# Kernel tuning notes

Measured on AMD Instinct MI355X. Metric: run time of the kernel, lower is better.

Reference implementation:

```python
import jax, jax.numpy as jnp
import numpy as np
import math

B, H, S, D = 4, 16, 1024, 64
NEG = -1000000000.0

def setup_inputs() -> dict:
    key = jax.random.key(0)
    ks = jax.random.split(key, 6)
    return {
        "query": jax.random.normal(ks[0], (B, H, S, D), dtype=jnp.float32),
        "key": jax.random.normal(ks[1], (B, H, S, D), dtype=jnp.float32),
        "value": jax.random.normal(ks[2], (B, H, S, D), dtype=jnp.float32),
        "head_nums": H,
        "mask": jax.random.randint(ks[3], (B, S), 0, 2, dtype=jnp.int32),
        "topic_query": jax.random.normal(ks[4], (B, S, D), dtype=jnp.float32),
        "topic_key": jax.random.normal(ks[5], (B, S, D), dtype=jnp.float32),
    }

def reference(query, key, value, head_nums, mask, topic_query, topic_key):
    d = query.shape[-1]
    # scores: [B,H,S,S]
    scores = jnp.einsum("bhqd,bhkd->bhqk", query, key) / math.sqrt(d)
    # pairwise mask: [B,S,S] (mask_i * mask_j)
    pair_mask = (mask[:, :, None] * mask[:, None, :]) != 0
    scores = jnp.where(pair_mask[:, None, :, :], scores, NEG)
    # topic modulation: per-token (no head dim), broadcast over heads
    dt = topic_query.shape[-1]
    topic_scores = jnp.einsum("bqd,bkd->bqk", topic_query, topic_key) / math.sqrt(dt)
    topic_scores = jnp.where(pair_mask, topic_scores, 1.0)[:, None, :, :]  # [B,1,S,S]
    topic_probs = jax.nn.softmax(topic_scores, axis=-1)
    scores = scores * topic_probs
    p_attn = jax.nn.softmax(scores, axis=-1)
    out = jnp.einsum("bhqk,bhkd->bhqd", p_attn, value)
    return (out, p_attn)
```

## Files before the change

### kernel.cpp

```cpp
#include <hip/hip_runtime.h>

#define B_ 4
#define H_ 16
#define S_ 1024
#define D_ 64
#define NEGV -1000000000.0f

typedef __bf16 bf16x8 __attribute__((ext_vector_type(8)));
typedef float f32x4 __attribute__((ext_vector_type(4)));

__global__ __launch_bounds__(256) void prep_kernel(
    const float* __restrict__ K, const float* __restrict__ V,
    __bf16* __restrict__ Kb, __bf16* __restrict__ Vt)
{
  int bid = blockIdx.x;
  int sc = bid & 15;
  int bh = bid >> 4;
  int tid = threadIdx.x;
  __shared__ float s_v[64][65];

  const float* Kc = K + ((size_t)bh*S_ + sc*64)*D_;
  const float* Vc = V + ((size_t)bh*S_ + sc*64)*D_;
  __bf16* Kbc = Kb + ((size_t)bh*S_ + sc*64)*D_;

  {
    const float4* src = (const float4*)Kc + tid*4;
    float4 a = src[0], b = src[1], c = src[2], d = src[3];
    bf16x8 o0, o1;
    o0[0]=(__bf16)a.x; o0[1]=(__bf16)a.y; o0[2]=(__bf16)a.z; o0[3]=(__bf16)a.w;
    o0[4]=(__bf16)b.x; o0[5]=(__bf16)b.y; o0[6]=(__bf16)b.z; o0[7]=(__bf16)b.w;
    o1[0]=(__bf16)c.x; o1[1]=(__bf16)c.y; o1[2]=(__bf16)c.z; o1[3]=(__bf16)c.w;
    o1[4]=(__bf16)d.x; o1[5]=(__bf16)d.y; o1[6]=(__bf16)d.z; o1[7]=(__bf16)d.w;
    *(bf16x8*)(Kbc + tid*16)     = o0;
    *(bf16x8*)(Kbc + tid*16 + 8) = o1;
  }
  for (int i = tid; i < 64*16; i += 256) {
    int r = i >> 4, c4 = i & 15;
    float4 v = ((const float4*)(Vc + (size_t)r*D_))[c4];
    s_v[r][c4*4+0] = v.x; s_v[r][c4*4+1] = v.y;
    s_v[r][c4*4+2] = v.z; s_v[r][c4*4+3] = v.w;
  }
  __syncthreads();
  {
    int d = tid >> 2, seg = tid & 3;
    bf16x8 o0, o1;
    #pragma unroll
    for (int j = 0; j < 8; ++j) o0[j] = (__bf16)s_v[seg*16 + j][d];
    #pragma unroll
    for (int j = 0; j < 8; ++j) o1[j] = (__bf16)s_v[seg*16 + 8 + j][d];
    __bf16* dst = Vt + ((size_t)bh*D_ + d)*S_ + sc*64 + seg*16;
    *(bf16x8*)dst = o0;
    *(bf16x8*)(dst + 8) = o1;
  }
}

__global__ __launch_bounds__(256) void topic_kernel(
    const float* __restrict__ tq, const float* __restrict__ tk,
    const int* __restrict__ mask, float* __restrict__ tp)
{
  int bid = blockIdx.x;
  int qt = bid & 63, b = bid >> 6;
  int tid = threadIdx.x;
  int wave = tid >> 6, lane = tid & 63;
  int l15 = lane & 15, lhi = lane >> 4;

  __shared__ float s_t[16*1024];

  bf16x8 qf[2];
  #pragma unroll
  for (int dc = 0; dc < 2; ++dc) {
    const float* p = tq + ((size_t)b*S_ + qt*16 + l15)*D_ + dc*32 + lhi*8;
    float4 x = *(const float4*)p;
    float4 y = *(const float4*)(p+4);
    bf16x8 f;
    f[0]=(__bf16)x.x; f[1]=(__bf16)x.y; f[2]=(__bf16)x.z; f[3]=(__bf16)x.w;
    f[4]=(__bf16)y.x; f[5]=(__bf16)y.y; f[6]=(__bf16)y.z; f[7]=(__bf16)y.w;
    qf[dc] = f;
  }
  int mq[4];
  #pragma unroll
  for (int i = 0; i < 4; ++i) mq[i] = mask[b*S_ + qt*16 + lhi*4 + i];

  for (int kt = 0; kt < 16; ++kt) {
    int kb = wave*256 + kt*16;
    int kcol = kb + l15;
    f32x4 acc = {0.f,0.f,0.f,0.f};
    #pragma unroll
    for (int dc = 0; dc < 2; ++dc) {
      const float* p = tk + ((size_t)b*S_ + kcol)*D_ + dc*32 + lhi*8;
      float4 x = *(const float4*)p;
      float4 y = *(const float4*)(p+4);
      bf16x8 f;
      f[0]=(__bf16)x.x; f[1]=(__bf16)x.y; f[2]=(__bf16)x.z; f[3]=(__bf16)x.w;
      f[4]=(__bf16)y.x; f[5]=(__bf16)y.y; f[6]=(__bf16)y.z; f[7]=(__bf16)y.w;
      acc = __builtin_amdgcn_mfma_f32_16x16x32_bf16(qf[dc], f, acc, 0, 0, 0);
    }
    int mk = mask[b*S_ + kcol];
    #pragma unroll
    for (int i = 0; i < 4; ++i) {
      int row = lhi*4 + i;
      float s = (mq[i] && mk) ? acc[i]*0.125f : 1.0f;
      s_t[row*1024 + (kcol ^ ((row&7)<<2))] = s;
    }
  }
  __syncthreads();

  int mkv[16];
  #pragma unroll
  for (int j = 0; j < 16; ++j) mkv[j] = mask[b*S_ + lane + j*64];
  int mqr[4];
  #pragma unroll
  for (int r = 0; r < 4; ++r) mqr[r] = mask[b*S_ + qt*16 + wave*4 + r];

  #pragma unroll
  for (int r = 0; r < 4; ++r) {
    int row = wave*4 + r;
    int swz = (row & 7) << 2;
    float sv[16]; float m = -3.4e38f;
    #pragma unroll
    for (int j = 0; j < 16; ++j) {
      sv[j] = s_t[row*1024 + ((lane + j*64) ^ swz)];
      m = fmaxf(m, sv[j]);
    }
    #pragma unroll
    for (int o = 32; o >= 1; o >>= 1) m = fmaxf(m, __shfl_xor(m, o));
    float ev[16]; float sum = 0.f;
    #pragma unroll
    for (int j = 0; j < 16; ++j) { ev[j] = __expf(sv[j]-m); sum += ev[j]; }
    #pragma unroll
    for (int o = 32; o >= 1; o >>= 1) sum += __shfl_xor(sum, o);
    float inv = 1.0f/sum;
    float* tpr = tp + ((size_t)b*S_ + qt*16 + row)*S_;
    #pragma unroll
    for (int j = 0; j < 16; ++j) {
      float p = ev[j]*inv;
      tpr[lane + j*64] = (mqr[r] && mkv[j]) ? p : -p;
    }
  }
}

__global__ __launch_bounds__(256) void attn_kernel(
    const float* __restrict__ Q, const __bf16* __restrict__ Kb,
    const __bf16* __restrict__ Vt, const float* __restrict__ tp,
    float* __restrict__ out, float* __restrict__ pa)
{
  int bid0 = blockIdx.x;
  int bid = (bid0 & 7)*512 + (bid0 >> 3);
  int qt = bid & 63;
  int h  = (bid >> 6) & 15;
  int b  = bid >> 10;
  int tid = threadIdx.x;
  int wave = tid >> 6, lane = tid & 63;
  int l15 = lane & 15, lhi = lane >> 4;

  __shared__ __bf16 s_p[16*1024];

  size_t bh = (size_t)b*H_ + h;
  const __bf16* Kbh = Kb + bh*S_*D_;
  const float* tpb = tp + ((size_t)b*S_ + qt*16)*S_;

  bf16x8 qf[2];
  #pragma unroll
  for (int dc = 0; dc < 2; ++dc) {
    const float* p = Q + (bh*S_ + qt*16 + l15)*D_ + dc*32 + lhi*8;
    float4 x = *(const float4*)p;
    float4 y = *(const float4*)(p+4);
    bf16x8 f;
    f[0]=(__bf16)x.x; f[1]=(__bf16)x.y; f[2]=(__bf16)x.z; f[3]=(__bf16)x.w;
    f[4]=(__bf16)y.x; f[5]=(__bf16)y.y; f[6]=(__bf16)y.z; f[7]=(__bf16)y.w;
    qf[dc] = f;
  }

  for (int kt = 0; kt < 16; ++kt) {
    int kb = wave*256 + kt*16;
    int kcol = kb + l15;
    const __bf16* kr = Kbh + (size_t)kcol*D_ + lhi*8;
    bf16x8 k0 = *(const bf16x8*)kr;
    bf16x8 k1 = *(const bf16x8*)(kr + 32);
    f32x4 acc = {0.f,0.f,0.f,0.f};
    acc = __builtin_amdgcn_mfma_f32_16x16x32_bf16(qf[0], k0, acc, 0, 0, 0);
    acc = __builtin_amdgcn_mfma_f32_16x16x32_bf16(qf[1], k1, acc, 0, 0, 0);
    #pragma unroll
    for (int i = 0; i < 4; ++i) {
      int row = lhi*4 + i;
      float t = tpb[(size_t)row*S_ + kcol];
      float at = fabsf(t);
      float s = (t > 0.f ? acc[i]*0.125f : NEGV) * at;
      *(__bf16*)((char*)s_p + row*2048 + (((kcol*2)) ^ ((row&7)<<4))) = (__bf16)s;
    }
  }
  __syncthreads();

  #pragma unroll
  for (int r = 0; r < 4; ++r) {
    int row = wave*4 + r;
    int swz = (row & 7) << 4;
    float sv[16]; float m = -3.4e38f;
    #pragma unroll
    for (int j = 0; j < 16; ++j) {
      sv[j] = (float)*(const __bf16*)((char*)s_p + row*2048 + (((lane + j*64)*2) ^ swz));
      m = fmaxf(m, sv[j]);
    }
    #pragma unroll
    for (int o = 32; o >= 1; o >>= 1) m = fmaxf(m, __shfl_xor(m, o));
    float ev[16]; float sum = 0.f;
    #pragma unroll
    for (int j = 0; j < 16; ++j) { ev[j] = __expf(sv[j]-m); sum += ev[j]; }
    #pragma unroll
    for (int o = 32; o >= 1; o >>= 1) sum += __shfl_xor(sum, o);
    float inv = 1.0f/sum;
    float* par = pa + (bh*S_ + qt*16 + row)*S_;
    #pragma unroll
    for (int j = 0; j < 16; ++j) {
      float p = ev[j]*inv;
      par[lane + j*64] = p;
      *(__bf16*)((char*)s_p + row*2048 + (((lane + j*64)*2) ^ swz)) = (__bf16)p;
    }
  }
  __syncthreads();

  const __bf16* Vh = Vt + (bh*D_ + wave*16 + l15)*S_ + lhi*8;
  f32x4 oacc = {0.f,0.f,0.f,0.f};
  #pragma unroll 8
  for (int ks = 0; ks < 32; ++ks) {
    bf16x8 a  = *(const bf16x8*)((char*)s_p + l15*2048 + (((ks*32 + lhi*8)*2) ^ ((l15&7)<<4)));
    bf16x8 bv = *(const bf16x8*)(Vh + ks*32);
    oacc = __builtin_amdgcn_mfma_f32_16x16x32_bf16(a, bv, oacc, 0, 0, 0);
  }
  #pragma unroll
  for (int i = 0; i < 4; ++i) {
    out[(bh*S_ + qt*16 + lhi*4 + i)*D_ + wave*16 + l15] = oacc[i];
  }
}

extern "C" void kernel_launch(void* const* d_in, const int* in_sizes, int n_in,
                              void* d_out, int out_size, void* d_ws, size_t ws_size,
                              hipStream_t stream) {
  const float* Q    = (const float*)d_in[0];
  const float* K    = (const float*)d_in[1];
  const float* V    = (const float*)d_in[2];
  const int*   mask = (const int*)d_in[4];
  const float* tq   = (const float*)d_in[5];
  const float* tk   = (const float*)d_in[6];

  float*  tp = (float*)d_ws;
  __bf16* Kb = (__bf16*)((char*)d_ws + (size_t)B_*S_*S_*4);
  __bf16* Vt = Kb + (size_t)B_*H_*S_*D_;

  float* outp = (float*)d_out;
  float* pa   = outp + (size_t)B_*H_*S_*D_;

  prep_kernel <<<B_*H_*16, 256, 0, stream>>>(K, V, Kb, Vt);
  topic_kernel<<<B_*64,    256, 0, stream>>>(tq, tk, mask, tp);
  attn_kernel <<<B_*H_*64, 256, 0, stream>>>(Q, Kb, Vt, tp, outp, pa);
}
```

Baseline: 190.9 us.

## Keep score tiles in registers with transposed MFMA and cross-wave softmax reduction

Both the topic and attention kernels now swap MFMA operands so each lane holds four consecutive key columns of one query row, keeping all scores in registers. Softmax statistics are combined across waves through a tiny shared-memory reduction instead of staging the full score matrix in LDS. This allows vectorized float4 reads of topic probabilities and vectorized, nontemporal stores of p_attn and out. The topic kernel's block order is also remapped. Register pressure rises (64 floats of scores per lane), which could lower occupancy.

```diff
diff --git a/kernel.cpp b/kernel.cpp
--- a/kernel.cpp
+++ b/kernel.cpp
@@ -7,7 +7,17 @@
 #define NEGV -1000000000.0f
 
 typedef __bf16 bf16x8 __attribute__((ext_vector_type(8)));
+typedef __bf16 bf16x4 __attribute__((ext_vector_type(4)));
 typedef float f32x4 __attribute__((ext_vector_type(4)));
+
+__device__ __forceinline__ bf16x8 cvt8(const float* p) {
+  float4 x = *(const float4*)p;
+  float4 y = *(const float4*)(p + 4);
+  bf16x8 f;
+  f[0]=(__bf16)x.x; f[1]=(__bf16)x.y; f[2]=(__bf16)x.z; f[3]=(__bf16)x.w;
+  f[4]=(__bf16)y.x; f[5]=(__bf16)y.y; f[6]=(__bf16)y.z; f[7]=(__bf16)y.w;
+  return f;
+}
 
 __global__ __launch_bounds__(256) void prep_kernel(
     const float* __restrict__ K, const float* __restrict__ V,
@@ -58,84 +68,73 @@
     const float* __restrict__ tq, const float* __restrict__ tk,
     const int* __restrict__ mask, float* __restrict__ tp)
 {
-  int bid = blockIdx.x;
+  int bid0 = blockIdx.x;
+  int bid = (bid0 & 7)*32 + (bid0 >> 3);
   int qt = bid & 63, b = bid >> 6;
-  int tid = threadIdx.x;
-  int wave = tid >> 6, lane = tid & 63;
+  int tid = threadIdx.x, wave = tid >> 6, lane = tid & 63;
   int l15 = lane & 15, lhi = lane >> 4;
-
-  __shared__ float s_t[16*1024];
-
+  __shared__ float2 s_red[4][16];
+
+  const int* mb = mask + b*S_;
   bf16x8 qf[2];
   #pragma unroll
-  for (int dc = 0; dc < 2; ++dc) {
-    const float* p = tq + ((size_t)b*S_ + qt*16 + l15)*D_ + dc*32 + lhi*8;
-    float4 x = *(const float4*)p;
-    float4 y = *(const float4*)(p+4);
-    bf16x8 f;
-    f[0]=(__bf16)x.x; f[1]=(__bf16)x.y; f[2]=(__bf16)x.z; f[3]=(__bf16)x.w;
-    f[4]=(__bf16)y.x; f[5]=(__bf16)y.y; f[6]=(__bf16)y.z; f[7]=(__bf16)y.w;
-    qf[dc] = f;
-  }
-  int mq[4];
-  #pragma unroll
-  for (int i = 0; i < 4; ++i) mq[i] = mask[b*S_ + qt*16 + lhi*4 + i];
-
-  for (int kt = 0; kt < 16; ++kt) {
-    int kb = wave*256 + kt*16;
-    int kcol = kb + l15;
+  for (int dc = 0; dc < 2; ++dc)
+    qf[dc] = cvt8(tq + ((size_t)b*S_ + qt*16 + l15)*D_ + dc*32 + lhi*8);
+  int mq = mb[qt*16 + l15];
+
+  f32x4 sc[16];
+  #pragma unroll
+  for (int kt = 0; kt < 16; ++kt) {
+    int kb = wave*256 + kt*16;
+    const float* kr = tk + ((size_t)b*S_ + kb + l15)*D_ + lhi*8;
+    bf16x8 k0 = cvt8(kr);
+    bf16x8 k1 = cvt8(kr + 32);
     f32x4 acc = {0.f,0.f,0.f,0.f};
-    #pragma unroll
-    for (int dc = 0; dc < 2; ++dc) {
-      const float* p = tk + ((size_t)b*S_ + kcol)*D_ + dc*32 + lhi*8;
-      float4 x = *(const float4*)p;
-      float4 y = *(const float4*)(p+4);
-      bf16x8 f;
-      f[0]=(__bf16)x.x; f[1]=(__bf16)x.y; f[2]=(__bf16)x.z; f[3]=(__bf16)x.w;
-      f[4]=(__bf16)y.x; f[5]=(__bf16)y.y; f[6]=(__bf16)y.z; f[7]=(__bf16)y.w;
-      acc = __builtin_amdgcn_mfma_f32_16x16x32_bf16(qf[dc], f, acc, 0, 0, 0);
-    }
-    int mk = mask[b*S_ + kcol];
-    #pragma unroll
-    for (int i = 0; i < 4; ++i) {
-      int row = lhi*4 + i;
-      float s = (mq[i] && mk) ? acc[i]*0.125f : 1.0f;
-      s_t[row*1024 + (kcol ^ ((row&7)<<2))] = s;
-    }
-  }
-  __syncthreads();
-
-  int mkv[16];
-  #pragma unroll
-  for (int j = 0; j < 16; ++j) mkv[j] = mask[b*S_ + lane + j*64];
-  int mqr[4];
-  #pragma unroll
-  for (int r = 0; r < 4; ++r) mqr[r] = mask[b*S_ + qt*16 + wave*4 + r];
-
-  #pragma unroll
-  for (int r = 0; r < 4; ++r) {
-    int row = wave*4 + r;
-    int swz = (row & 7) << 2;
-    float sv[16]; float m = -3.4e38f;
-    #pragma unroll
-    for (int j = 0; j < 16; ++j) {
-      sv[j] = s_t[row*1024 + ((lane + j*64) ^ swz)];
-      m = fmaxf(m, sv[j]);
-    }
-    #pragma unroll
-    for (int o = 32; o >= 1; o >>= 1) m = fmaxf(m, __shfl_xor(m, o));
-    float ev[16]; float sum = 0.f;
-    #pragma unroll
-    for (int j = 0; j < 16; ++j) { ev[j] = __expf(sv[j]-m); sum += ev[j]; }
-    #pragma unroll
-    for (int o = 32; o >= 1; o >>= 1) sum += __shfl_xor(sum, o);
-    float inv = 1.0f/sum;
-    float* tpr = tp + ((size_t)b*S_ + qt*16 + row)*S_;
-    #pragma unroll
-    for (int j = 0; j < 16; ++j) {
-      float p = ev[j]*inv;
-      tpr[lane + j*64] = (mqr[r] && mkv[j]) ? p : -p;
-    }
+    acc = __builtin_amdgcn_mfma_f32_16x16x32_bf16(k0, qf[0], acc, 0, 0, 0);
+    acc = __builtin_amdgcn_mfma_f32_16x16x32_bf16(k1, qf[1], acc, 0, 0, 0);
+    int4 mk = *(const int4*)(mb + kb + lhi*4);
+    sc[kt][0] = (mq && mk.x) ? acc[0]*0.125f : 1.0f;
+    sc[kt][1] = (mq && mk.y) ? acc[1]*0.125f : 1.0f;
+    sc[kt][2] = (mq && mk.z) ? acc[2]*0.125f : 1.0f;
+    sc[kt][3] = (mq && mk.w) ? acc[3]*0.125f : 1.0f;
+  }
+  float m = -3.4e38f;
+  #pragma unroll
+  for (int kt = 0; kt < 16; ++kt) {
+    #pragma unroll
+    for (int i = 0; i < 4; ++i) m = fmaxf(m, sc[kt][i]);
+  }
+  m = fmaxf(m, __shfl_xor(m, 16));
+  m = fmaxf(m, __shfl_xor(m, 32));
+  float sum = 0.f;
+  #pragma unroll
+  for (int kt = 0; kt < 16; ++kt) {
+    #pragma unroll
+    for (int i = 0; i < 4; ++i) { sc[kt][i] = __expf(sc[kt][i] - m); sum += sc[kt][i]; }
+  }
+  sum += __shfl_xor(sum, 16);
+  sum += __shfl_xor(sum, 32);
+  if (lane < 16) s_red[wave][l15] = make_float2(m, sum);
+  __syncthreads();
+  float M = -3.4e38f;
+  #pragma unroll
+  for (int w = 0; w < 4; ++w) M = fmaxf(M, s_red[w][l15].x);
+  float Z = 0.f;
+  #pragma unroll
+  for (int w = 0; w < 4; ++w) Z += s_red[w][l15].y * __expf(s_red[w][l15].x - M);
+  float scale = __expf(m - M) / Z;
+
+  float* tpr = tp + ((size_t)b*S_ + qt*16 + l15)*S_;
+  #pragma unroll
+  for (int kt = 0; kt < 16; ++kt) {
+    int kb = wave*256 + kt*16;
+    int4 mk = *(const int4*)(mb + kb + lhi*4);
+    f32x4 pv;
+    pv[0] = sc[kt][0]*scale; if (!(mq && mk.x)) pv[0] = -pv[0];
+    pv[1] = sc[kt][1]*scale; if (!(mq && mk.y)) pv[1] = -pv[1];
+    pv[2] = sc[kt][2]*scale; if (!(mq && mk.z)) pv[2] = -pv[2];
+    pv[3] = sc[kt][3]*scale; if (!(mq && mk.w)) pv[3] = -pv[3];
+    *(f32x4*)(tpr + kb + lhi*4) = pv;
   }
 }
 
@@ -149,88 +148,92 @@
   int qt = bid & 63;
   int h  = (bid >> 6) & 15;
   int b  = bid >> 10;
-  int tid = threadIdx.x;
-  int wave = tid >> 6, lane = tid & 63;
+  int tid = threadIdx.x, wave = tid >> 6, lane = tid & 63;
   int l15 = lane & 15, lhi = lane >> 4;
 
   __shared__ __bf16 s_p[16*1024];
+  __shared__ float2 s_red[4][16];
 
   size_t bh = (size_t)b*H_ + h;
   const __bf16* Kbh = Kb + bh*S_*D_;
-  const float* tpb = tp + ((size_t)b*S_ + qt*16)*S_;
+  const float* tpb = tp + ((size_t)b*S_ + qt*16 + l15)*S_;
 
   bf16x8 qf[2];
   #pragma unroll
-  for (int dc = 0; dc < 2; ++dc) {
-    const float* p = Q + (bh*S_ + qt*16 + l15)*D_ + dc*32 + lhi*8;
-    float4 x = *(const float4*)p;
-    float4 y = *(const float4*)(p+4);
-    bf16x8 f;
-    f[0]=(__bf16)x.x; f[1]=(__bf16)x.y; f[2]=(__bf16)x.z; f[3]=(__bf16)x.w;
-    f[4]=(__bf16)y.x; f[5]=(__bf16)y.y; f[6]=(__bf16)y.z; f[7]=(__bf16)y.w;
-    qf[dc] = f;
-  }
-
-  for (int kt = 0; kt < 16; ++kt) {
-    int kb = wave*256 + kt*16;
-    int kcol = kb + l15;
-    const __bf16* kr = Kbh + (size_t)kcol*D_ + lhi*8;
+  for (int dc = 0; dc < 2; ++dc)
+    qf[dc] = cvt8(Q + (bh*S_ + qt*16 + l15)*D_ + dc*32 + lhi*8);
+
+  f32x4 sc[16];
+  #pragma unroll
+  for (int kt = 0; kt < 16; ++kt) {
+    int kb = wave*256 + kt*16;
+    const __bf16* kr = Kbh + (size_t)(kb + l15)*D_ + lhi*8;
     bf16x8 k0 = *(const bf16x8*)kr;
     bf16x8 k1 = *(const bf16x8*)(kr + 32);
     f32x4 acc = {0.f,0.f,0.f,0.f};
-    acc = __builtin_amdgcn_mfma_f32_16x16x32_bf16(qf[0], k0, acc, 0, 0, 0);
-    acc = __builtin_amdgcn_mfma_f32_16x16x32_bf16(qf[1], k1, acc, 0, 0, 0);
-    #pragma unroll
-    for (int i = 0; i < 4; ++i) {
-      int row = lhi*4 + i;
-      float t = tpb[(size_t)row*S_ + kcol];
-      float at = fabsf(t);
-      float s = (t > 0.f ? acc[i]*0.125f : NEGV) * at;
-      *(__bf16*)((char*)s_p + row*2048 + (((kcol*2)) ^ ((row&7)<<4))) = (__bf16)s;
-    }
-  }
-  __syncthreads();
-
-  #pragma unroll
-  for (int r = 0; r < 4; ++r) {
-    int row = wave*4 + r;
-    int swz = (row & 7) << 4;
-    float sv[16]; float m = -3.4e38f;
-    #pragma unroll
-    for (int j = 0; j < 16; ++j) {
-      sv[j] = (float)*(const __bf16*)((char*)s_p + row*2048 + (((lane + j*64)*2) ^ swz));
-      m = fmaxf(m, sv[j]);
-    }
-    #pragma unroll
-    for (int o = 32; o >= 1; o >>= 1) m = fmaxf(m, __shfl_xor(m, o));
-    float ev[16]; float sum = 0.f;
-    #pragma unroll
-    for (int j = 0; j < 16; ++j) { ev[j] = __expf(sv[j]-m); sum += ev[j]; }
-    #pragma unroll
-    for (int o = 32; o >= 1; o >>= 1) sum += __shfl_xor(sum, o);
-    float inv = 1.0f/sum;
-    float* par = pa + (bh*S_ + qt*16 + row)*S_;
-    #pragma unroll
-    for (int j = 0; j < 16; ++j) {
-      float p = ev[j]*inv;
-      par[lane + j*64] = p;
-      *(__bf16*)((char*)s_p + row*2048 + (((lane + j*64)*2) ^ swz)) = (__bf16)p;
-    }
+    acc = __builtin_amdgcn_mfma_f32_16x16x32_bf16(k0, qf[0], acc, 0, 0, 0);
+    acc = __builtin_amdgcn_mfma_f32_16x16x32_bf16(k1, qf[1], acc, 0, 0, 0);
+    float4 t = *(const float4*)(tpb + kb + lhi*4);
+    sc[kt][0] = (t.x > 0.f) ? acc[0]*0.125f*t.x : NEGV*(-t.x);
+    sc[kt][1] = (t.y > 0.f) ? acc[1]*0.125f*t.y : NEGV*(-t.y);
+    sc[kt][2] = (t.z > 0.f) ? acc[2]*0.125f*t.z : NEGV*(-t.z);
+    sc[kt][3] = (t.w > 0.f) ? acc[3]*0.125f*t.w : NEGV*(-t.w);
+  }
+
+  float m = -3.4e38f;
+  #pragma unroll
+  for (int kt = 0; kt < 16; ++kt) {
+    #pragma unroll
+    for (int i = 0; i < 4; ++i) m = fmaxf(m, sc[kt][i]);
+  }
+  m = fmaxf(m, __shfl_xor(m, 16));
+  m = fmaxf(m, __shfl_xor(m, 32));
+  float sum = 0.f;
+  #pragma unroll
+  for (int kt = 0; kt < 16; ++kt) {
+    #pragma unroll
+    for (int i = 0; i < 4; ++i) { sc[kt][i] = __expf(sc[kt][i] - m); sum += sc[kt][i]; }
+  }
+  sum += __shfl_xor(sum, 16);
+  sum += __shfl_xor(sum, 32);
+  if (lane < 16) s_red[wave][l15] = make_float2(m, sum);
+  __syncthreads();
+  float M = -3.4e38f;
+  #pragma unroll
+  for (int w = 0; w < 4; ++w) M = fmaxf(M, s_red[w][l15].x);
+  float Z = 0.f;
+  #pragma unroll
+  for (int w = 0; w < 4; ++w) Z += s_red[w][l15].y * __expf(s_red[w][l15].x - M);
+  float scale = __expf(m - M) / Z;
+
+  float* par = pa + (bh*S_ + qt*16 + l15)*S_;
+  #pragma unroll
+  for (int kt = 0; kt < 16; ++kt) {
+    int kb = wave*256 + kt*16;
+    f32x4 pv;
+    pv[0] = sc[kt][0]*scale;
+    pv[1] = sc[kt][1]*scale;
+    pv[2] = sc[kt][2]*scale;
+    pv[3] = sc[kt][3]*scale;
+    __builtin_nontemporal_store(pv, (f32x4*)(par + kb + lhi*4));
+    bf16x4 pb;
+    pb[0] = (__bf16)pv[0]; pb[1] = (__bf16)pv[1];
+    pb[2] = (__bf16)pv[2]; pb[3] = (__bf16)pv[3];
+    *(bf16x4*)((char*)s_p + l15*2048 + ((wave*512 + kt*32 + lhi*8) ^ ((l15 & 7) << 4))) = pb;
   }
   __syncthreads();
 
   const __bf16* Vh = Vt + (bh*D_ + wave*16 + l15)*S_ + lhi*8;
   f32x4 oacc = {0.f,0.f,0.f,0.f};
-  #pragma unroll 8
+  #pragma unroll
   for (int ks = 0; ks < 32; ++ks) {
-    bf16x8 a  = *(const bf16x8*)((char*)s_p + l15*2048 + (((ks*32 + lhi*8)*2) ^ ((l15&7)<<4)));
+    bf16x8 a  = *(const bf16x8*)((char*)s_p + l15*2048 + ((ks*64 + lhi*16) ^ ((l15 & 7) << 4)));
     bf16x8 bv = *(const bf16x8*)(Vh + ks*32);
     oacc = __builtin_amdgcn_mfma_f32_16x16x32_bf16(a, bv, oacc, 0, 0, 0);
   }
   #pragma unroll
-  for (int i = 0; i < 4; ++i) {
-    out[(bh*S_ + qt*16 + lhi*4 + i)*D_ + wave*16 + l15] = oacc[i];
-  }
+  for (int i = 0; i < 4; ++i)
+    __builtin_nontemporal_store(oacc[i], out + (bh*S_ + qt*16 + lhi*4 + i)*D_ + wave*16 + l15);
 }
 
 extern "C" void kernel_launch(void* const* d_in, const int* in_sizes, int n_in,
```

Result: slower. 209.9 us (+10.0%).
